# Kernel optimization log

Hardware: AMD Instinct MI355X
Metric: run time of the kernel (lower is better)

## Reference

```python
import jax, jax.numpy as jnp
import numpy as np

ORDER = 4          # signature truncation depth
SCALAR_TERM = True # leading 1 term, as in signatory.signature(..., scalar_term=True)
BATCH, STREAM, CHAN = 2048, 128, 5  # channel = path_dim + 1 (time + 4-dim path)


def _exp_levels(dx, m):
    """Tensor exponential of a single increment dx: levels dx^{(x)k}/k!, k=1..m.
    dx: (B, d). Returns list of (B, d**k) arrays."""
    levels = [dx]
    for k in range(2, m + 1):
        prev = levels[-1]  # (B, d**(k-1))
        levels.append((prev[:, :, None] * dx[:, None, :]).reshape(dx.shape[0], -1) / k)
    return levels


def _chen(S, E):
    """Chen's identity: (S tensor-multiply E) truncated to depth m.
    S, E: tuples/lists of (B, d**k) level arrays (level k at list index k-1)."""
    m = len(E)
    B = E[0].shape[0]
    out = []
    for k in range(m):  # output level k+1
        term = S[k] + E[k]
        for i in range(k):  # S level (i+1) tensor E level (k-i)
            a, b = S[i], E[k - 1 - i]
            term = term + (a[:, :, None] * b[:, None, :]).reshape(B, -1)
        out.append(term)
    return tuple(out)


def _signature(path, m, scalar_term):
    """Truncated path signature, flattened levels 1..m (optionally with leading 1).
    path: (B, T, d) -> (B, [1+] d + d^2 + ... + d^m)."""
    B, T, d = path.shape
    dx = jnp.moveaxis(path[:, 1:] - path[:, :-1], 1, 0)  # (T-1, B, d)
    init = tuple(jnp.zeros((B, d ** k), path.dtype) for k in range(1, m + 1))

    def step(S, inc):
        return _chen(S, _exp_levels(inc, m)), None

    S, _ = jax.lax.scan(step, init, dx)
    sig = jnp.concatenate(S, axis=1)
    if scalar_term:
        sig = jnp.concatenate([jnp.ones((B, 1), path.dtype), sig], axis=1)
    return sig


def setup_inputs() -> dict:
    key = jax.random.key(0)
    kx, ky = jax.random.split(key)
    x = jax.random.normal(kx, (BATCH, STREAM, CHAN), dtype=jnp.float32)
    y = jax.random.normal(ky, (BATCH, STREAM, CHAN), dtype=jnp.float32)
    sigma = jnp.ones((CHAN - 1,), dtype=jnp.float32)  # adversarial scaling params
    return {"x": x, "y": y, "sigma": sigma}


def reference(x, y, sigma):
    # adversarial scaling applied to x's non-time channels only (as in forward())
    mu = jnp.concatenate([x[..., :1], x[..., 1:] * sigma], axis=-1)
    nu = y
    # signatures computed once each and shared across kxx, kxy, kyy (same math)
    sx = _signature(mu, ORDER, SCALAR_TERM)  # (B, P)
    sy = _signature(nu, ORDER, SCALAR_TERM)  # (B, P)
    kxx = jnp.einsum('ip,jp->ij', sx, sx)
    kxy = jnp.einsum('ip,jp->ij', sx, sy)
    kyy = jnp.einsum('ip,jp->ij', sy, sy)
    return jnp.mean(kxx) - 2.0 * jnp.mean(kxy) + jnp.mean(kyy)
```

## Files before the change

kernel.cpp:

```cpp
#include <hip/hip_runtime.h>

typedef float v2f __attribute__((ext_vector_type(2)));

#define BATCH  2048
#define TLEN   128
#define CH     5
#define SIGDIM 780
#define KACC   16
#define PPB    4
#define NBLK   ((2 * BATCH) / PPB)
#define SEGR   64
#define POISON 0xAAAAAAAAu

__global__ __launch_bounds__(256, 4) void sig_kernel(
    const float* __restrict__ x, const float* __restrict__ y,
    const float* __restrict__ sigma, float* __restrict__ acc,
    unsigned int* __restrict__ counter, float* __restrict__ out) {
  const int tid  = threadIdx.x;
  const int wave = tid >> 6;
  const int lane = tid & 63;
  const int h    = lane >> 5;
  const int u    = lane & 31;
  const bool isX = (blockIdx.x < NBLK / 2);
  const int pbase = (isX ? blockIdx.x : blockIdx.x - NBLK / 2) * PPB;
  const int path  = pbase + wave;
  const float* src = (isX ? x : y) + (size_t)path * (TLEN * CH) + h * (SEGR * CH);

  __shared__ __align__(16) float buf[2 * PPB][784];
  __shared__ float blockAcc[SIGDIM];
  __shared__ float red[4];
  __shared__ unsigned int lastFlag;

  for (int i = tid; i < SIGDIM; i += 256) blockAcc[i] = 0.f;

  const float sg0 = sigma[0], sg1 = sigma[1], sg2 = sigma[2], sg3 = sigma[3];

  float* bw = buf[wave * 2 + h];
  if (h == 1 && u < 8) bw[63 * 8 + u] = 0.f;
  const int lim = h ? 63 * CH : 64 * CH;
  for (int i = u; i < lim; i += 32) {
    int t = i / CH, c = i - CH * t;
    float v = src[i + CH] - src[i];
    if (isX && c > 0) {
      const float s = (c == 1) ? sg0 : (c == 2) ? sg1 : (c == 3) ? sg2 : sg3;
      v *= s;
    }
    bw[t * 8 + c] = v;
  }
  __syncthreads();

  const int  uc = u < 25 ? u : 24;
  const int  a_ = uc / 5, b_ = uc - 5 * a_;
  const bool act = (u < 25);

  float s1a = 0.f, s2 = 0.f;
  v2f   s3p0 = {0.f, 0.f}, s3p1 = {0.f, 0.f};
  float s3e = 0.f;
  v2f   s4p0[5] = {{0,0},{0,0},{0,0},{0,0},{0,0}};
  v2f   s4p1[5] = {{0,0},{0,0},{0,0},{0,0},{0,0}};
  float s4e[5]  = {0,0,0,0,0};

  const float* pa_ = bw + a_;
  const float* pb_ = bw + b_;

  for (int g = 0; g < 8; ++g) {
    const float* rg = bw + g * 64;
    const float* ra = pa_ + g * 64;
    const float* rb = pb_ + g * 64;
    #pragma unroll
    for (int k = 0; k < 8; ++k) {
      const float4 m = *(const float4*)(rg + k * 8);
      const float d0 = m.x, d1 = m.y, d2 = m.z, d3 = m.w;
      const float d4 = rg[k * 8 + 4];
      const float da = ra[k * 8];
      const float db = rb[k * 8];
      const float pa = s1a * (1.f / 6.f) + da * (1.f / 24.f);
      const float qa = s1a * 0.5f        + da * (1.f / 6.f);
      const float rr = s1a               + da * 0.5f;
      s1a += da;
      const float p2 = 0.5f * s2 + db * pa;
      const float q2 =        s2 + db * qa;
      s2 += db * rr;
      const v2f dc01 = {d0, d1};
      const v2f dc23 = {d2, d3};
      const v2f p2v  = {p2, p2};
      const v2f q2v  = {q2, q2};
      const v2f p30  = __builtin_elementwise_fma(dc01, p2v, s3p0);
      const v2f p31  = __builtin_elementwise_fma(dc23, p2v, s3p1);
      const float p3e = s3e + d4 * p2;
      s3p0 = __builtin_elementwise_fma(dc01, q2v, s3p0);
      s3p1 = __builtin_elementwise_fma(dc23, q2v, s3p1);
      s3e += d4 * q2;
      #pragma unroll
      for (int d = 0; d < 5; ++d) {
        const float dd = (d == 0) ? d0 : (d == 1) ? d1 : (d == 2) ? d2 : (d == 3) ? d3 : d4;
        const v2f ddv = {dd, dd};
        s4p0[d] = __builtin_elementwise_fma(ddv, p30, s4p0[d]);
        s4p1[d] = __builtin_elementwise_fma(ddv, p31, s4p1[d]);
        s4e[d] += dd * p3e;
      }
    }
  }

  float S3[5] = {s3p0.x, s3p0.y, s3p1.x, s3p1.y, s3e};
  float S4[5][5];
  #pragma unroll
  for (int d = 0; d < 5; ++d) {
    S4[0][d] = s4p0[d].x; S4[1][d] = s4p0[d].y;
    S4[2][d] = s4p1[d].x; S4[3][d] = s4p1[d].y;
    S4[4][d] = s4e[d];
  }

  if (h == 1 && act) {
    float* sgb = bw;
    if (b_ == 0) sgb[a_] = s1a;
    sgb[5 + uc] = s2;
    #pragma unroll
    for (int c = 0; c < 5; ++c) {
      sgb[30 + uc * 5 + c] = S3[c];
      #pragma unroll
      for (int d = 0; d < 5; ++d) sgb[155 + (uc * 5 + c) * 5 + d] = S4[c][d];
    }
  }
  __syncthreads();

  if (h == 0 && act) {
    const float* R = buf[wave * 2 + 1];
    const float o1 = s1a + R[a_];
    const float o2 = s2 + s1a * R[b_] + R[5 + uc];
    if (b_ == 0) atomicAdd(&blockAcc[a_], o1);
    atomicAdd(&blockAcc[5 + uc], o2);
    #pragma unroll
    for (int c = 0; c < 5; ++c) {
      const float o3 = S3[c] + s2 * R[c] + s1a * R[5 + b_ * 5 + c] + R[30 + uc * 5 + c];
      atomicAdd(&blockAcc[30 + uc * 5 + c], o3);
      #pragma unroll
      for (int d = 0; d < 5; ++d) {
        const float o4 = S4[c][d] + S3[c] * R[d] + s2 * R[5 + c * 5 + d]
                       + s1a * R[30 + (b_ * 5 + c) * 5 + d]
                       + R[155 + (uc * 5 + c) * 5 + d];
        atomicAdd(&blockAcc[155 + (uc * 5 + c) * 5 + d], o4);
      }
    }
  }
  __syncthreads();

  const float w = isX ? 1.0f : -1.0f;
  float* ap = acc + (size_t)(blockIdx.x & (KACC - 1)) * SIGDIM;
  for (int i = tid; i < SIGDIM; i += 256)
    atomicAdd(ap + i, w * blockAcc[i]);

  __syncthreads();
  if (tid == 0) {
    __threadfence();
    unsigned int old = __hip_atomic_fetch_add(counter, 1u, __ATOMIC_ACQ_REL,
                                              __HIP_MEMORY_SCOPE_AGENT);
    lastFlag = (old == POISON + (NBLK - 1)) ? 1u : 0u;
  }
  __syncthreads();
  if (lastFlag) {
    float local = 0.f;
    for (int i = tid; i < SIGDIM; i += 256) {
      float v = 0.f;
      #pragma unroll
      for (int k = 0; k < KACC; ++k)
        v += __hip_atomic_load(&acc[(size_t)k * SIGDIM + i],
                               __ATOMIC_RELAXED, __HIP_MEMORY_SCOPE_AGENT);
      local += v * v;
    }
    #pragma unroll
    for (int off = 32; off > 0; off >>= 1) local += __shfl_down(local, off, 64);
    if ((tid & 63) == 0) red[tid >> 6] = local;
    __syncthreads();
    if (tid == 0)
      out[0] = (red[0] + red[1] + red[2] + red[3]) / (2048.0f * 2048.0f);
  }
}

extern "C" void kernel_launch(void* const* d_in, const int* in_sizes, int n_in,
                              void* d_out, int out_size, void* d_ws, size_t ws_size,
                              hipStream_t stream) {
  const float* x     = (const float*)d_in[0];
  const float* y     = (const float*)d_in[1];
  const float* sigma = (const float*)d_in[2];
  float* out = (float*)d_out;
  float* acc = (float*)d_ws;
  unsigned int* counter = (unsigned int*)((char*)d_ws + (size_t)KACC * SIGDIM * sizeof(float));

  sig_kernel<<<dim3(NBLK), dim3(256), 0, stream>>>(x, y, sigma, acc, counter, out);
}
```

Baseline: 106.8 us.

## Replace global atomic accumulation with per-block partials and separate reduction kernel

Each signature block now writes its weighted partial signature sum to its own row in the workspace, instead of issuing atomicAdds into 16 shared accumulator copies. A new 16-block reduction kernel sums those rows, combines them atomically into one accumulator, and the last block computes the squared-norm output. This removes the contended global atomics and the last-block counter from the main kernel. In exchange it adds a second kernel launch and a 3.2 MB round trip of partial results through memory.

```diff
diff --git a/kernel.cpp b/kernel.cpp
--- a/kernel.cpp
+++ b/kernel.cpp
@@ -6,16 +6,15 @@
 #define TLEN   128
 #define CH     5
 #define SIGDIM 780
-#define KACC   16
 #define PPB    4
 #define NBLK   ((2 * BATCH) / PPB)
 #define SEGR   64
+#define RBLK   16
 #define POISON 0xAAAAAAAAu
 
 __global__ __launch_bounds__(256, 4) void sig_kernel(
     const float* __restrict__ x, const float* __restrict__ y,
-    const float* __restrict__ sigma, float* __restrict__ acc,
-    unsigned int* __restrict__ counter, float* __restrict__ out) {
+    const float* __restrict__ sigma, float* __restrict__ part) {
   const int tid  = threadIdx.x;
   const int wave = tid >> 6;
   const int lane = tid & 63;
@@ -28,8 +27,6 @@
 
   __shared__ __align__(16) float buf[2 * PPB][784];
   __shared__ float blockAcc[SIGDIM];
-  __shared__ float red[4];
-  __shared__ unsigned int lastFlag;
 
   for (int i = tid; i < SIGDIM; i += 256) blockAcc[i] = 0.f;
 
@@ -146,26 +143,44 @@
   __syncthreads();
 
   const float w = isX ? 1.0f : -1.0f;
-  float* ap = acc + (size_t)(blockIdx.x & (KACC - 1)) * SIGDIM;
-  for (int i = tid; i < SIGDIM; i += 256)
-    atomicAdd(ap + i, w * blockAcc[i]);
-
+  float* pp = part + (size_t)blockIdx.x * SIGDIM;
+  for (int i = tid; i < SIGDIM; i += 256) pp[i] = w * blockAcc[i];
+}
+
+__global__ __launch_bounds__(256) void red_kernel(
+    const float* __restrict__ part, float* __restrict__ acc2,
+    unsigned int* __restrict__ counter, float* __restrict__ out) {
+  const int tid = threadIdx.x;
+  float r0 = 0.f, r1 = 0.f, r2 = 0.f, r3 = 0.f;
+  const int c0 = tid, c1 = tid + 256, c2 = tid + 512, c3 = tid + 768;
+  const int rbase = blockIdx.x * (NBLK / RBLK);
+  for (int rr = 0; rr < NBLK / RBLK; ++rr) {
+    const float* row = part + (size_t)(rbase + rr) * SIGDIM;
+    r0 += row[c0];
+    if (c1 < SIGDIM) r1 += row[c1];
+    if (c2 < SIGDIM) r2 += row[c2];
+    if (c3 < SIGDIM) r3 += row[c3];
+  }
+  atomicAdd(&acc2[c0], r0);
+  if (c1 < SIGDIM) atomicAdd(&acc2[c1], r1);
+  if (c2 < SIGDIM) atomicAdd(&acc2[c2], r2);
+  if (c3 < SIGDIM) atomicAdd(&acc2[c3], r3);
+
+  __shared__ float red[4];
+  __shared__ unsigned int lastFlag;
   __syncthreads();
   if (tid == 0) {
     __threadfence();
     unsigned int old = __hip_atomic_fetch_add(counter, 1u, __ATOMIC_ACQ_REL,
                                               __HIP_MEMORY_SCOPE_AGENT);
-    lastFlag = (old == POISON + (NBLK - 1)) ? 1u : 0u;
+    lastFlag = (old == POISON + (RBLK - 1)) ? 1u : 0u;
   }
   __syncthreads();
   if (lastFlag) {
     float local = 0.f;
     for (int i = tid; i < SIGDIM; i += 256) {
-      float v = 0.f;
-      #pragma unroll
-      for (int k = 0; k < KACC; ++k)
-        v += __hip_atomic_load(&acc[(size_t)k * SIGDIM + i],
-                               __ATOMIC_RELAXED, __HIP_MEMORY_SCOPE_AGENT);
+      float v = __hip_atomic_load(&acc2[i], __ATOMIC_RELAXED,
+                                  __HIP_MEMORY_SCOPE_AGENT);
       local += v * v;
     }
     #pragma unroll
@@ -184,8 +199,12 @@
   const float* y     = (const float*)d_in[1];
   const float* sigma = (const float*)d_in[2];
   float* out = (float*)d_out;
-  float* acc = (float*)d_ws;
-  unsigned int* counter = (unsigned int*)((char*)d_ws + (size_t)KACC * SIGDIM * sizeof(float));
-
-  sig_kernel<<<dim3(NBLK), dim3(256), 0, stream>>>(x, y, sigma, acc, counter, out);
+  float* part = (float*)d_ws;
+  float* acc2 = (float*)((char*)d_ws + (size_t)NBLK * SIGDIM * sizeof(float));
+  unsigned int* counter =
+      (unsigned int*)((char*)d_ws + (size_t)NBLK * SIGDIM * sizeof(float)
+                      + SIGDIM * sizeof(float));
+
+  sig_kernel<<<dim3(NBLK), dim3(256), 0, stream>>>(x, y, sigma, part);
+  red_kernel<<<dim3(RBLK), dim3(256), 0, stream>>>(part, acc2, counter, out);
 }
```

Measured after the change: 143.0 us. 1.34x slower.
